# Optimization experiments

Measured on AMD Instinct MI355X. Metric: run time of the kernel, lower is better.

## Reference

```python
import jax, jax.numpy as jnp
import numpy as np

B, S, D, H = 2, 4096, 128, 128
EPS = 1e-6
NEG_INF = -1e30


def _complex_linear(xr, xi, Wr, Wi, br, bi):
    # x: (B,S,D); W: (H,D); complex linear (Wr + i Wi)(xr + i xi) + (br + i bi) per layer math:
    # real_out = (xr Wr + br) - (xi Wi + bi); imag_out = (xi Wr + br) + (xr Wi + bi)
    out_r = xr @ Wr.T + br - (xi @ Wi.T + bi)
    out_i = xi @ Wr.T + br + (xr @ Wi.T + bi)
    return out_r, out_i


def setup_inputs() -> dict:
    key = jax.random.key(0)
    ks = jax.random.split(key, 24)
    scale = 1.0 / np.sqrt(D)
    def W(k):
        return jax.random.normal(k, (H, D), jnp.float32) * scale
    def b(k):
        return jax.random.normal(k, (H,), jnp.float32) * 0.01
    inp = {
        "Z_q": jax.random.normal(ks[0], (B, 2, S, D, 1), jnp.float32),
        "Z_k": jax.random.normal(ks[1], (B, 2, S, D, 1), jnp.float32),
        "Z_v": jax.random.normal(ks[2], (B, 2, S, D, 1), jnp.float32),
        "Wq_r": W(ks[3]), "Wq_i": W(ks[4]), "bq_r": b(ks[5]), "bq_i": b(ks[6]),
        "Wk_r": W(ks[7]), "Wk_i": W(ks[8]), "bk_r": b(ks[9]), "bk_i": b(ks[10]),
        "Wv_r": W(ks[11]), "Wv_i": W(ks[12]), "bv_r": b(ks[13]), "bv_i": b(ks[14]),
        "Wp_r": W(ks[15]), "Wp_i": W(ks[16]), "bp_r": b(ks[17]), "bp_i": b(ks[18]),
        "noise_floor": jnp.asarray(1.0, jnp.float32),
        "tau": jnp.asarray(0.0, jnp.float32),
    }
    return inp


def reference(Z_q, Z_k, Z_v,
              Wq_r, Wq_i, bq_r, bq_i,
              Wk_r, Wk_i, bk_r, bk_i,
              Wv_r, Wv_i, bv_r, bv_i,
              Wp_r, Wp_i, bp_r, bp_i,
              noise_floor, tau):
    # squeeze trailing singleton; split real/imag -> (B,S,D)
    zqr, zqi = Z_q[:, 0, :, :, 0], Z_q[:, 1, :, :, 0]
    zkr, zki = Z_k[:, 0, :, :, 0], Z_k[:, 1, :, :, 0]
    zvr, zvi = Z_v[:, 0, :, :, 0], Z_v[:, 1, :, :, 0]

    Qr, Qi = _complex_linear(zqr, zqi, Wq_r, Wq_i, bq_r, bq_i)
    Kr, Ki = _complex_linear(zkr, zki, Wk_r, Wk_i, bk_r, bk_i)
    Vr, Vi = _complex_linear(zvr, zvi, Wv_r, Wv_i, bv_r, bv_i)

    # InverseMahalanobis: R2[b,i,j] = sum_h |Q[b,i]-K[b,j]|^2
    q2 = jnp.sum(Qr * Qr + Qi * Qi, axis=-1)          # (B,S)
    k2 = jnp.sum(Kr * Kr + Ki * Ki, axis=-1)          # (B,S)
    re_qk = (jnp.einsum('bsh,bth->bst', Qr, Kr)
             + jnp.einsum('bsh,bth->bst', Qi, Ki))    # (B,S,S)
    R2 = q2[:, :, None] + k2[:, None, :] - 2.0 * re_qk

    attn_scores = -jax.nn.softplus(tau) * jnp.log(noise_floor ** 2 + R2 + EPS)
    mask = jnp.tril(jnp.ones((S, S), dtype=bool))[None]
    attn_scores = jnp.where(mask, attn_scores, NEG_INF)
    attn_weights = jax.nn.softmax(attn_scores / jnp.sqrt(jnp.float32(H)), axis=-1)

    # attn (real) times complex V
    est_r = jnp.einsum('bst,bth->bsh', attn_weights, Vr)
    est_i = jnp.einsum('bst,bth->bsh', attn_weights, Vi)

    out_r, out_i = _complex_linear(est_r, est_i, Wp_r, Wp_i, bp_r, bp_i)
    out = jnp.stack((out_r, out_i), axis=1)[..., None]  # (B,2,S,H,1)
    return out, attn_weights
```

## Files before the change

kernel.cpp:

```cpp
#include <hip/hip_runtime.h>

#define S_LEN 4096
#define NBATCH 2
#define ROWS (NBATCH*S_LEN)
#define OUT_ELEMS 2097152

typedef _Float16 f16;
typedef _Float16 f16x8 __attribute__((ext_vector_type(8)));
typedef _Float16 f16x4 __attribute__((ext_vector_type(4)));
typedef float f32x4 __attribute__((ext_vector_type(4)));

#define MT_OFF    0x000000
#define BIAS_OFF  0x080000
#define SC_OFF    0x081000
#define QH_OFF    0x100000
#define KH_OFF    0x500000
#define VT_OFF    0x900000
#define Q2_OFF    0xD00000
#define K2_OFF    0xD10000
#define L_OFF     0xD20000
#define EST_OFF   0xE00000
#define WS_NEED   0x1600000

#define MFMA16(A,B,C) __builtin_amdgcn_mfma_f32_16x16x32_f16(A,B,C,0,0,0)

__device__ __forceinline__ void async_cp16(f16* lds, const f16* g) {
  __builtin_amdgcn_global_load_lds(
      (const __attribute__((address_space(1))) void*)g,
      (__attribute__((address_space(3))) void*)lds, 16, 0, 0);
}

__device__ __forceinline__ void stage16(f16* lds, const f16* g, int stride, int tid) {
#pragma unroll
  for (int i = 0; i < 2; ++i) {
    int idx = i*256 + tid;
    int row = idx >> 2, c = idx & 3;
    async_cp16(lds + idx*8, g + (size_t)row*stride + c*8);
  }
}

__device__ __forceinline__ void stage32(f16* lds, const float* g, int stride, int tid) {
#pragma unroll
  for (int i = 0; i < 4; ++i) {
    int idx = i*256 + tid;
    int row = idx >> 3, c = idx & 7;
    const float4* gp = (const float4*)(g + (size_t)row*stride + c*4);
    float4 v = *gp;
    f16x4 h; h[0]=(f16)v.x; h[1]=(f16)v.y; h[2]=(f16)v.z; h[3]=(f16)v.w;
    *(f16x4*)(lds + row*32 + c*4) = h;
  }
}

__device__ __forceinline__ void mfma_step(const f16* Asm, const f16* Bsm, int lane,
                                          int wm, int wn, f32x4 acc[4][4]) {
  f16x8 a[4], b[4];
  int rr = lane & 15, kk = (lane >> 4) << 3;
#pragma unroll
  for (int i=0;i<4;i++) a[i] = *(const f16x8*)(Asm + (wm + i*16 + rr)*32 + kk);
#pragma unroll
  for (int j=0;j<4;j++) b[j] = *(const f16x8*)(Bsm + (wn + j*16 + rr)*32 + kk);
#pragma unroll
  for (int i=0;i<4;i++)
#pragma unroll
    for (int j=0;j<4;j++) acc[i][j] = MFMA16(a[i], b[j], acc[i][j]);
}

__global__ __launch_bounds__(256)
void k_build(const float* Wqr, const float* Wqi, const float* bqr, const float* bqi,
             const float* Wkr, const float* Wki, const float* bkr, const float* bki,
             const float* Wvr, const float* Wvi, const float* bvr, const float* bvi,
             const float* Wpr, const float* Wpi, const float* bpr, const float* bpi,
             f16* Mt, float* bias) {
  int mat = blockIdx.x;
  const float *Wr, *Wi, *br, *bi;
  if (mat == 0)      { Wr=Wqr; Wi=Wqi; br=bqr; bi=bqi; }
  else if (mat == 1) { Wr=Wkr; Wi=Wki; br=bkr; bi=bki; }
  else if (mat == 2) { Wr=Wvr; Wi=Wvi; br=bvr; bi=bvi; }
  else               { Wr=Wpr; Wi=Wpi; br=bpr; bi=bpi; }
  int idx = blockIdx.y*256 + threadIdx.x;
  int n = idx >> 8, k = idx & 255;
  int d = k & 127, h = n & 127;
  float w = (k < 128) ? ((n < 128) ? Wr[h*128+d] : Wi[h*128+d])
                      : ((n < 128) ? -Wi[h*128+d] : Wr[h*128+d]);
  Mt[mat*65536 + n*256 + k] = (f16)w;
  if (k == 0)
    bias[mat*256 + n] = (n < 128) ? (br[n] - bi[n]) : (br[n-128] + bi[n-128]);
}

__global__ __launch_bounds__(256)
void k_init(float* est, float* lsum, float* sc, const float* nf, const float* tau) {
  int idx = blockIdx.x*256 + threadIdx.x;
  if (idx < 524288) ((float4*)est)[idx] = make_float4(0.f,0.f,0.f,0.f);
  else { int j = idx - 524288; if (j < 2048) ((float4*)lsum)[j] = make_float4(0.f,0.f,0.f,0.f); }
  if (idx == 0) {
    float t = tau[0];
    float c = __builtin_log2f(1.0f + __builtin_exp2f(t * 1.4426950408889634f))
              * 0.6931471805599453f;
    sc[0] = -c * 0.08838834764831845f;
    sc[1] = nf[0]*nf[0] + 1e-6f;
  }
}

__global__ __launch_bounds__(256)
void k_proj(const float* Zq, const float* Zk, const float* Zv,
            const f16* Mt, const float* bias,
            f16* Qh, f16* Kh, f16* Vt) {
  __shared__ f16 Asm[128*32];
  __shared__ f16 Bsm[128*32];
  __shared__ float bias_s[128];
  int tid = threadIdx.x;
  int mode = blockIdx.z;
  int m0 = blockIdx.x * 128, n0 = blockIdx.y * 128;
  const float* Z = (mode==0) ? Zq : (mode==1 ? Zk : Zv);
  const f16* Bt = Mt + mode*65536;
  if (tid < 128) bias_s[tid] = bias[mode*256 + n0 + tid];
  int b = m0 >> 12, s0 = m0 & 4095;
  int lane = tid & 63, w = tid >> 6;
  int wm = (w >> 1)*64, wn = (w & 1)*64;
  f32x4 acc[4][4] = {};
  for (int kb = 0; kb < 8; ++kb) {
    int k0 = kb*32;
    int part = k0 >> 7, d0 = k0 & 127;
    const float* Ag = Z + (((size_t)(b*2 + part))*S_LEN + s0)*128 + d0;
    stage32(Asm, Ag, 128, tid);
    stage16(Bsm, Bt + n0*256 + k0, 256, tid);
    __syncthreads();
    mfma_step(Asm, Bsm, lane, wm, wn, acc);
    __syncthreads();
  }
  int rr = (lane>>4)*4, cc = lane & 15;
  if (mode < 2) {
    f16* O = (mode==0) ? Qh : Kh;
#pragma unroll
    for (int i=0;i<4;i++)
#pragma unroll
      for (int j=0;j<4;j++) {
        int cl = wn + j*16 + cc;
        int cg = n0 + cl;
        float bv = bias_s[cl];
#pragma unroll
        for (int r=0;r<4;r++) {
          int rg = m0 + wm + i*16 + rr + r;
          O[(size_t)rg*256 + cg] = (f16)(acc[i][j][r] + bv);
        }
      }
  } else {
#pragma unroll
    for (int i=0;i<4;i++) {
      int t0 = s0 + wm + i*16 + rr;
#pragma unroll
      for (int j=0;j<4;j++) {
        int cl = wn + j*16 + cc;
        int cg = n0 + cl;
        float bv = bias_s[cl];
        f16x4 h4;
#pragma unroll
        for (int r=0;r<4;r++) h4[r] = (f16)(acc[i][j][r] + bv);
        *(f16x4*)(Vt + (size_t)b*1048576 + (size_t)cg*4096 + t0) = h4;
      }
    }
  }
}

__global__ __launch_bounds__(256)
void k_sq(const f16* Qh, const f16* Kh, float* q2, float* k2) {
  int w = threadIdx.x >> 6, lane = threadIdx.x & 63;
  int rid = blockIdx.x*4 + w;
  const f16* src = (rid < ROWS) ? Qh + (size_t)rid*256 : Kh + (size_t)(rid-ROWS)*256;
  f16x4 v = *(const f16x4*)(src + lane*4);
  float s = 0.f;
#pragma unroll
  for (int i=0;i<4;i++) { float f = (float)v[i]; s += f*f; }
#pragma unroll
  for (int m=32;m>=1;m>>=1) s += __shfl_xor(s, m, 64);
  if (lane==0) { if (rid < ROWS) q2[rid]=s; else k2[rid-ROWS]=s; }
}

template<int WRITE>
__global__ __launch_bounds__(256)
void k_attn(const f16* Qh, const f16* Kh, const float* q2, const float* k2,
            const float* sc, float* lsum, float* attn) {
  __shared__ f16 Asm[128*32];
  __shared__ f16 Bsm[128*32];
  __shared__ float q2s[128], k2s[128], ls[128];
  int x = blockIdx.x;
  int b = x / 528, r = x % 528;
  int sb = (int)((__builtin_sqrtf(8.f*(float)r + 1.f) - 1.f)*0.5f);
  while ((sb+1)*(sb+2)/2 <= r) sb++;
  while (sb*(sb+1)/2 > r) sb--;
  int tb = r - sb*(sb+1)/2;
  int s0 = sb*128, t0 = tb*128;
  int tid = threadIdx.x;
  if (tid < 128) {
    q2s[tid] = q2[b*S_LEN + s0 + tid];
    k2s[tid] = k2[b*S_LEN + t0 + tid];
    if (WRITE) ls[tid] = 1.0f / lsum[b*S_LEN + s0 + tid];
  }
  float kc = sc[0], nf2 = sc[1];
  int lane = tid & 63, w = tid >> 6;
  int wm = (w >> 1)*64, wn = (w & 1)*64;
  const f16* Ag = Qh + ((size_t)(b*S_LEN) + s0)*256;
  const f16* Bg = Kh + ((size_t)(b*S_LEN) + t0)*256;
  f32x4 acc[4][4] = {};
  for (int kb=0;kb<8;kb++) {
    stage16(Asm, Ag + kb*32, 256, tid);
    stage16(Bsm, Bg + kb*32, 256, tid);
    __syncthreads();
    mfma_step(Asm, Bsm, lane, wm, wn, acc);
    __syncthreads();
  }
  int rr = (lane>>4)*4, cc = lane & 15;
  bool diag = (tb == sb);
  if (WRITE) {
#pragma unroll
    for (int i=0;i<4;i++)
#pragma unroll
      for (int j=0;j<4;j++) {
        int cl = wn + j*16 + cc;
        float kv = k2s[cl];
#pragma unroll
        for (int rg=0;rg<4;rg++) {
          int rl = wm + i*16 + rr + rg;
          float xx = nf2 + q2s[rl] + kv - 2.0f*acc[i][j][rg];
          float P = __builtin_exp2f(kc * __builtin_log2f(__builtin_fmaxf(xx, 1e-6f)));
          if (diag && (t0+cl) > (s0+rl)) P = 0.f;
          attn[((size_t)(b*S_LEN) + s0 + rl)*S_LEN + t0 + cl] = P * ls[rl];
        }
      }
  } else {
    float rs[4][4];
#pragma unroll
    for (int i=0;i<4;i++)
#pragma unroll
      for (int rg=0;rg<4;rg++) rs[i][rg]=0.f;
#pragma unroll
    for (int i=0;i<4;i++)
#pragma unroll
      for (int j=0;j<4;j++) {
        int cl = wn + j*16 + cc;
        float kv = k2s[cl];
#pragma unroll
        for (int rg=0;rg<4;rg++) {
          int rl = wm + i*16 + rr + rg;
          float xx = nf2 + q2s[rl] + kv - 2.0f*acc[i][j][rg];
          float P = __builtin_exp2f(kc * __builtin_log2f(__builtin_fmaxf(xx, 1e-6f)));
          if (diag && (t0+cl) > (s0+rl)) P = 0.f;
          rs[i][rg] += P;
        }
      }
#pragma unroll
    for (int m=8;m>=1;m>>=1)
#pragma unroll
      for (int i=0;i<4;i++)
#pragma unroll
        for (int rg=0;rg<4;rg++) rs[i][rg] += __shfl_xor(rs[i][rg], m, 64);
    if (cc == 0)
#pragma unroll
      for (int i=0;i<4;i++)
#pragma unroll
        for (int rg=0;rg<4;rg++) {
          int rl = wm + i*16 + rr + rg;
          atomicAdd(&lsum[b*S_LEN + s0 + rl], rs[i][rg]);
        }
  }
}

__global__ __launch_bounds__(256)
void k_zupper(float* attn) {
  int rid = blockIdx.x;
  int b = rid >> 12, s = rid & 4095;
  int tstart = ((s >> 7) + 1) << 7;
  float4* p = (float4*)(attn + ((size_t)(b*S_LEN) + s)*S_LEN);
  for (int i = (tstart >> 2) + threadIdx.x; i < 1024; i += 256)
    p[i] = make_float4(0.f,0.f,0.f,0.f);
}

__global__ __launch_bounds__(256)
void k_pv(const float* attn, const f16* Vt, float* est) {
  __shared__ f16 Asm[128*32];
  __shared__ f16 Bsm[128*32];
  int sb = blockIdx.x, nb = blockIdx.y, z = blockIdx.z;
  int b = z >> 2, tc = z & 3;
  if (tc > (sb >> 3)) return;
  int s0 = sb*128, h0 = nb*128;
  int tid = threadIdx.x;
  int lane = tid & 63, w = tid >> 6;
  int wm = (w>>1)*64, wn = (w&1)*64;
  int tb1 = tc*8 + 8; if (tb1 > sb+1) tb1 = sb+1;
  const float* Abase = attn + ((size_t)(b*S_LEN) + s0)*S_LEN;
  const f16* Bbase = Vt + (size_t)b*1048576 + (size_t)h0*4096;
  f32x4 acc[4][4] = {};
  for (int tb = tc*8; tb < tb1; ++tb)
    for (int kk = 0; kk < 4; ++kk) {
      int t0 = tb*128 + kk*32;
      stage32(Asm, Abase + t0, S_LEN, tid);
      stage16(Bsm, Bbase + t0, 4096, tid);
      __syncthreads();
      mfma_step(Asm, Bsm, lane, wm, wn, acc);
      __syncthreads();
    }
  int rr = (lane>>4)*4, cc = lane & 15;
#pragma unroll
  for (int i=0;i<4;i++)
#pragma unroll
    for (int j=0;j<4;j++) {
      int cg = h0 + wn + j*16 + cc;
#pragma unroll
      for (int rg=0;rg<4;rg++) {
        int rgl = s0 + wm + i*16 + rr + rg;
        atomicAdd(&est[((size_t)(b*S_LEN) + rgl)*256 + cg], acc[i][j][rg]);
      }
    }
}

__global__ __launch_bounds__(256)
void k_out(const float* est, const f16* Mt, const float* bias, float* outp) {
  __shared__ f16 Asm[128*32];
  __shared__ f16 Bsm[128*32];
  __shared__ float bias_s[128];
  int m0 = blockIdx.x*128, n0 = blockIdx.y*128;
  int tid = threadIdx.x;
  if (tid < 128) bias_s[tid] = bias[3*256 + n0 + tid];
  int lane = tid & 63, w = tid >> 6;
  int wm = (w>>1)*64, wn = (w&1)*64;
  const f16* Bt = Mt + 3*65536;
  f32x4 acc[4][4] = {};
  for (int kb=0;kb<8;kb++) {
    stage32(Asm, est + (size_t)m0*256 + kb*32, 256, tid);
    stage16(Bsm, Bt + n0*256 + kb*32, 256, tid);
    __syncthreads();
    mfma_step(Asm, Bsm, lane, wm, wn, acc);
    __syncthreads();
  }
  int rr = (lane>>4)*4, cc = lane & 15;
  int b = m0 >> 12, s0 = m0 & 4095;
#pragma unroll
  for (int i=0;i<4;i++)
#pragma unroll
    for (int j=0;j<4;j++) {
      int cl = wn + j*16 + cc;
      int cg = n0 + cl;
      int comp = cg >> 7, h = cg & 127;
      float bv = bias_s[cl];
#pragma unroll
      for (int rg=0;rg<4;rg++) {
        int s = s0 + wm + i*16 + rr + rg;
        outp[(((size_t)(b*2 + comp))*S_LEN + s)*128 + h] = acc[i][j][rg] + bv;
      }
    }
}

extern "C" void kernel_launch(void* const* d_in, const int* in_sizes, int n_in,
                              void* d_out, int out_size, void* d_ws, size_t ws_size,
                              hipStream_t stream) {
  (void)in_sizes; (void)n_in; (void)out_size;
  if (ws_size < (size_t)WS_NEED) return;
  const float* Zq = (const float*)d_in[0];
  const float* Zk = (const float*)d_in[1];
  const float* Zv = (const float*)d_in[2];
  char* ws = (char*)d_ws;
  f16*   Mt   = (f16*)(ws + MT_OFF);
  float* bias = (float*)(ws + BIAS_OFF);
  float* sc   = (float*)(ws + SC_OFF);
  f16*   Qh   = (f16*)(ws + QH_OFF);
  f16*   Kh   = (f16*)(ws + KH_OFF);
  f16*   Vt   = (f16*)(ws + VT_OFF);
  float* q2   = (float*)(ws + Q2_OFF);
  float* k2   = (float*)(ws + K2_OFF);
  float* lsum = (float*)(ws + L_OFF);
  float* est  = (float*)(ws + EST_OFF);
  float* outp = (float*)d_out;
  float* attn = outp + OUT_ELEMS;

  k_build<<<dim3(4,256), 256, 0, stream>>>(
      (const float*)d_in[3],  (const float*)d_in[4],  (const float*)d_in[5],  (const float*)d_in[6],
      (const float*)d_in[7],  (const float*)d_in[8],  (const float*)d_in[9],  (const float*)d_in[10],
      (const float*)d_in[11], (const float*)d_in[12], (const float*)d_in[13], (const float*)d_in[14],
      (const float*)d_in[15], (const float*)d_in[16], (const float*)d_in[17], (const float*)d_in[18],
      Mt, bias);
  k_init<<<2056, 256, 0, stream>>>(est, lsum, sc, (const float*)d_in[19], (const float*)d_in[20]);
  k_proj<<<dim3(64,2,3), 256, 0, stream>>>(Zq, Zk, Zv, Mt, bias, Qh, Kh, Vt);
  k_sq<<<4096, 256, 0, stream>>>(Qh, Kh, q2, k2);
  k_attn<0><<<1056, 256, 0, stream>>>(Qh, Kh, q2, k2, sc, lsum, attn);
  k_attn<1><<<1056, 256, 0, stream>>>(Qh, Kh, q2, k2, sc, lsum, attn);
  k_zupper<<<8192, 256, 0, stream>>>(attn);
  k_pv<<<dim3(32,2,8), 256, 0, stream>>>(attn, Vt, est);
  k_out<<<dim3(64,2), 256, 0, stream>>>(est, Mt, bias, outp);
}
```

Before: 319.2 us.

## Single-pass attention with fp16 P workspace, fused normalization and zero-fill

Replaces the two-pass attention (sum pass plus recompute-and-write pass) with a single pass that writes unnormalized fp16 probabilities to a workspace and accumulates row sums. The PV kernel reads the fp16 P, writes the normalized fp32 attention output during staging, and the output projection applies the 1/lsum row scale. It also folds the q2/k2 norm computation into the projection epilogue via atomics and zero-fills the upper triangle inside the attention kernel. This removes one full QK^T recompute and halves the P read bandwidth, at the cost of a 64 MB workspace write/read and fp16 rounding of P before normalization.

```diff
diff --git a/kernel.cpp b/kernel.cpp
--- a/kernel.cpp
+++ b/kernel.cpp
@@ -20,7 +20,8 @@
 #define K2_OFF    0xD10000
 #define L_OFF     0xD20000
 #define EST_OFF   0xE00000
-#define WS_NEED   0x1600000
+#define PW_OFF    0x1600000
+#define WS_NEED   0x5600000
 
 #define MFMA16(A,B,C) __builtin_amdgcn_mfma_f32_16x16x32_f16(A,B,C,0,0,0)
 
@@ -39,14 +40,16 @@
   }
 }
 
-__device__ __forceinline__ void stage32(f16* lds, const float* g, int stride, int tid) {
+__device__ __forceinline__ void stage32(f16* lds, const float* g, int stride, int tid,
+                                        const float* rowscale) {
 #pragma unroll
   for (int i = 0; i < 4; ++i) {
     int idx = i*256 + tid;
     int row = idx >> 3, c = idx & 7;
     const float4* gp = (const float4*)(g + (size_t)row*stride + c*4);
     float4 v = *gp;
-    f16x4 h; h[0]=(f16)v.x; h[1]=(f16)v.y; h[2]=(f16)v.z; h[3]=(f16)v.w;
+    float sc = rowscale ? rowscale[row] : 1.0f;
+    f16x4 h; h[0]=(f16)(v.x*sc); h[1]=(f16)(v.y*sc); h[2]=(f16)(v.z*sc); h[3]=(f16)(v.w*sc);
     *(f16x4*)(lds + row*32 + c*4) = h;
   }
 }
@@ -88,10 +91,10 @@
 }
 
 __global__ __launch_bounds__(256)
-void k_init(float* est, float* lsum, float* sc, const float* nf, const float* tau) {
+void k_init(float* est, float* zreg, float* sc, const float* nf, const float* tau) {
   int idx = blockIdx.x*256 + threadIdx.x;
   if (idx < 524288) ((float4*)est)[idx] = make_float4(0.f,0.f,0.f,0.f);
-  else { int j = idx - 524288; if (j < 2048) ((float4*)lsum)[j] = make_float4(0.f,0.f,0.f,0.f); }
+  else { int j = idx - 524288; if (j < 12288) ((float4*)zreg)[j] = make_float4(0.f,0.f,0.f,0.f); }
   if (idx == 0) {
     float t = tau[0];
     float c = __builtin_log2f(1.0f + __builtin_exp2f(t * 1.4426950408889634f))
@@ -104,7 +107,7 @@
 __global__ __launch_bounds__(256)
 void k_proj(const float* Zq, const float* Zk, const float* Zv,
             const f16* Mt, const float* bias,
-            f16* Qh, f16* Kh, f16* Vt) {
+            f16* Qh, f16* Kh, f16* Vt, float* q2, float* k2) {
   __shared__ f16 Asm[128*32];
   __shared__ f16 Bsm[128*32];
   __shared__ float bias_s[128];
@@ -122,7 +125,7 @@
     int k0 = kb*32;
     int part = k0 >> 7, d0 = k0 & 127;
     const float* Ag = Z + (((size_t)(b*2 + part))*S_LEN + s0)*128 + d0;
-    stage32(Asm, Ag, 128, tid);
+    stage32(Asm, Ag, 128, tid, nullptr);
     stage16(Bsm, Bt + n0*256 + k0, 256, tid);
     __syncthreads();
     mfma_step(Asm, Bsm, lane, wm, wn, acc);
@@ -131,6 +134,11 @@
   int rr = (lane>>4)*4, cc = lane & 15;
   if (mode < 2) {
     f16* O = (mode==0) ? Qh : Kh;
+    float rs[4][4];
+#pragma unroll
+    for (int i=0;i<4;i++)
+#pragma unroll
+      for (int r=0;r<4;r++) rs[i][r]=0.f;
 #pragma unroll
     for (int i=0;i<4;i++)
 #pragma unroll
@@ -141,9 +149,28 @@
 #pragma unroll
         for (int r=0;r<4;r++) {
           int rg = m0 + wm + i*16 + rr + r;
-          O[(size_t)rg*256 + cg] = (f16)(acc[i][j][r] + bv);
+          f16 hv = (f16)(acc[i][j][r] + bv);
+          O[(size_t)rg*256 + cg] = hv;
+          float fv = (float)hv;
+          rs[i][r] += fv*fv;
         }
       }
+#pragma unroll
+    for (int m=8;m>=1;m>>=1)
+#pragma unroll
+      for (int i=0;i<4;i++)
+#pragma unroll
+        for (int r=0;r<4;r++) rs[i][r] += __shfl_xor(rs[i][r], m, 64);
+    if (cc == 0) {
+      float* T = (mode==0) ? q2 : k2;
+#pragma unroll
+      for (int i=0;i<4;i++)
+#pragma unroll
+        for (int r=0;r<4;r++) {
+          int rg = m0 + wm + i*16 + rr + r;
+          atomicAdd(&T[rg], rs[i][r]);
+        }
+    }
   } else {
 #pragma unroll
     for (int i=0;i<4;i++) {
@@ -163,38 +190,27 @@
 }
 
 __global__ __launch_bounds__(256)
-void k_sq(const f16* Qh, const f16* Kh, float* q2, float* k2) {
-  int w = threadIdx.x >> 6, lane = threadIdx.x & 63;
-  int rid = blockIdx.x*4 + w;
-  const f16* src = (rid < ROWS) ? Qh + (size_t)rid*256 : Kh + (size_t)(rid-ROWS)*256;
-  f16x4 v = *(const f16x4*)(src + lane*4);
-  float s = 0.f;
-#pragma unroll
-  for (int i=0;i<4;i++) { float f = (float)v[i]; s += f*f; }
-#pragma unroll
-  for (int m=32;m>=1;m>>=1) s += __shfl_xor(s, m, 64);
-  if (lane==0) { if (rid < ROWS) q2[rid]=s; else k2[rid-ROWS]=s; }
-}
-
-template<int WRITE>
-__global__ __launch_bounds__(256)
 void k_attn(const f16* Qh, const f16* Kh, const float* q2, const float* k2,
-            const float* sc, float* lsum, float* attn) {
+            const float* sc, float* lsum, f16* Pws, float* attn) {
+  int x = blockIdx.x;
+  int b = x >> 10, r = x & 1023;
+  int sb = r >> 5, tb = r & 31;
+  int s0 = sb*128, t0 = tb*128;
+  int tid = threadIdx.x;
+  if (tb > sb) {
+    float4 z = make_float4(0.f,0.f,0.f,0.f);
+    int row = tid >> 1, h = tid & 1;
+    float4* p = (float4*)(attn + ((size_t)(b*S_LEN) + s0 + row)*S_LEN + t0 + h*64);
+#pragma unroll
+    for (int i=0;i<16;i++) p[i] = z;
+    return;
+  }
   __shared__ f16 Asm[128*32];
   __shared__ f16 Bsm[128*32];
-  __shared__ float q2s[128], k2s[128], ls[128];
-  int x = blockIdx.x;
-  int b = x / 528, r = x % 528;
-  int sb = (int)((__builtin_sqrtf(8.f*(float)r + 1.f) - 1.f)*0.5f);
-  while ((sb+1)*(sb+2)/2 <= r) sb++;
-  while (sb*(sb+1)/2 > r) sb--;
-  int tb = r - sb*(sb+1)/2;
-  int s0 = sb*128, t0 = tb*128;
-  int tid = threadIdx.x;
+  __shared__ float q2s[128], k2s[128];
   if (tid < 128) {
     q2s[tid] = q2[b*S_LEN + s0 + tid];
     k2s[tid] = k2[b*S_LEN + t0 + tid];
-    if (WRITE) ls[tid] = 1.0f / lsum[b*S_LEN + s0 + tid];
   }
   float kc = sc[0], nf2 = sc[1];
   int lane = tid & 63, w = tid >> 6;
@@ -211,91 +227,81 @@
   }
   int rr = (lane>>4)*4, cc = lane & 15;
   bool diag = (tb == sb);
-  if (WRITE) {
+  float rs[4][4];
+#pragma unroll
+  for (int i=0;i<4;i++)
+#pragma unroll
+    for (int rg=0;rg<4;rg++) rs[i][rg]=0.f;
+#pragma unroll
+  for (int i=0;i<4;i++)
+#pragma unroll
+    for (int j=0;j<4;j++) {
+      int cl = wn + j*16 + cc;
+      float kv = k2s[cl];
+#pragma unroll
+      for (int rg=0;rg<4;rg++) {
+        int rl = wm + i*16 + rr + rg;
+        float xx = nf2 + q2s[rl] + kv - 2.0f*acc[i][j][rg];
+        float P = __builtin_exp2f(kc * __builtin_log2f(__builtin_fmaxf(xx, 1e-6f)));
+        if (diag && (t0+cl) > (s0+rl)) P = 0.f;
+        Pws[((size_t)(b*S_LEN) + s0 + rl)*S_LEN + t0 + cl] = (f16)P;
+        rs[i][rg] += P;
+      }
+    }
+#pragma unroll
+  for (int m=8;m>=1;m>>=1)
 #pragma unroll
     for (int i=0;i<4;i++)
 #pragma unroll
-      for (int j=0;j<4;j++) {
-        int cl = wn + j*16 + cc;
-        float kv = k2s[cl];
-#pragma unroll
-        for (int rg=0;rg<4;rg++) {
-          int rl = wm + i*16 + rr + rg;
-          float xx = nf2 + q2s[rl] + kv - 2.0f*acc[i][j][rg];
-          float P = __builtin_exp2f(kc * __builtin_log2f(__builtin_fmaxf(xx, 1e-6f)));
-          if (diag && (t0+cl) > (s0+rl)) P = 0.f;
-          attn[((size_t)(b*S_LEN) + s0 + rl)*S_LEN + t0 + cl] = P * ls[rl];
-        }
-      }
-  } else {
-    float rs[4][4];
+      for (int rg=0;rg<4;rg++) rs[i][rg] += __shfl_xor(rs[i][rg], m, 64);
+  if (cc == 0)
 #pragma unroll
     for (int i=0;i<4;i++)
 #pragma unroll
-      for (int rg=0;rg<4;rg++) rs[i][rg]=0.f;
-#pragma unroll
-    for (int i=0;i<4;i++)
-#pragma unroll
-      for (int j=0;j<4;j++) {
-        int cl = wn + j*16 + cc;
-        float kv = k2s[cl];
-#pragma unroll
-        for (int rg=0;rg<4;rg++) {
-          int rl = wm + i*16 + rr + rg;
-          float xx = nf2 + q2s[rl] + kv - 2.0f*acc[i][j][rg];
-          float P = __builtin_exp2f(kc * __builtin_log2f(__builtin_fmaxf(xx, 1e-6f)));
-          if (diag && (t0+cl) > (s0+rl)) P = 0.f;
-          rs[i][rg] += P;
-        }
-      }
-#pragma unroll
-    for (int m=8;m>=1;m>>=1)
-#pragma unroll
-      for (int i=0;i<4;i++)
-#pragma unroll
-        for (int rg=0;rg<4;rg++) rs[i][rg] += __shfl_xor(rs[i][rg], m, 64);
-    if (cc == 0)
-#pragma unroll
-      for (int i=0;i<4;i++)
-#pragma unroll
-        for (int rg=0;rg<4;rg++) {
-          int rl = wm + i*16 + rr + rg;
-          atomicAdd(&lsum[b*S_LEN + s0 + rl], rs[i][rg]);
-        }
-  }
-}
-
-__global__ __launch_bounds__(256)
-void k_zupper(float* attn) {
-  int rid = blockIdx.x;
-  int b = rid >> 12, s = rid & 4095;
-  int tstart = ((s >> 7) + 1) << 7;
-  float4* p = (float4*)(attn + ((size_t)(b*S_LEN) + s)*S_LEN);
-  for (int i = (tstart >> 2) + threadIdx.x; i < 1024; i += 256)
-    p[i] = make_float4(0.f,0.f,0.f,0.f);
-}
-
-__global__ __launch_bounds__(256)
-void k_pv(const float* attn, const f16* Vt, float* est) {
+      for (int rg=0;rg<4;rg++) {
+        int rl = wm + i*16 + rr + rg;
+        atomicAdd(&lsum[b*S_LEN + s0 + rl], rs[i][rg]);
+      }
+}
+
+__global__ __launch_bounds__(256)
+void k_pv(const f16* Pws, const f16* Vt, const float* lsum, float* est, float* attn) {
   __shared__ f16 Asm[128*32];
   __shared__ f16 Bsm[128*32];
-  int sb = blockIdx.x, nb = blockIdx.y, z = blockIdx.z;
-  int b = z >> 2, tc = z & 3;
-  if (tc > (sb >> 3)) return;
+  __shared__ float ls[128];
+  int r = blockIdx.x;
+  int nb = blockIdx.y, b = blockIdx.z;
+  int sb = 0;
+  while (r >= ((sb+4)>>2)) { r -= (sb+4)>>2; sb++; }
+  int c = r;
   int s0 = sb*128, h0 = nb*128;
   int tid = threadIdx.x;
+  bool wrb = (nb == 0);
+  if (wrb && tid < 128) ls[tid] = 1.0f / lsum[b*S_LEN + s0 + tid];
   int lane = tid & 63, w = tid >> 6;
   int wm = (w>>1)*64, wn = (w&1)*64;
-  int tb1 = tc*8 + 8; if (tb1 > sb+1) tb1 = sb+1;
-  const float* Abase = attn + ((size_t)(b*S_LEN) + s0)*S_LEN;
+  int tb0 = c*4, tb1 = tb0 + 4; if (tb1 > sb+1) tb1 = sb+1;
+  const f16* Abase = Pws + ((size_t)(b*S_LEN) + s0)*S_LEN;
   const f16* Bbase = Vt + (size_t)b*1048576 + (size_t)h0*4096;
   f32x4 acc[4][4] = {};
-  for (int tb = tc*8; tb < tb1; ++tb)
+  int row2 = tid >> 1, half2 = tid & 1;
+  for (int tb = tb0; tb < tb1; ++tb)
     for (int kk = 0; kk < 4; ++kk) {
       int t0 = tb*128 + kk*32;
-      stage32(Asm, Abase + t0, S_LEN, tid);
+      stage16(Asm, Abase + t0, S_LEN, tid);
       stage16(Bsm, Bbase + t0, 4096, tid);
       __syncthreads();
+      if (wrb) {
+        float invl = ls[row2];
+        const f16x8* src = (const f16x8*)(Asm + row2*32 + half2*16);
+        f16x8 v0 = src[0], v1 = src[1];
+        float4* dst = (float4*)(attn + ((size_t)(b*S_LEN) + s0 + row2)*S_LEN + t0 + half2*16);
+        float4 o;
+        o.x=(float)v0[0]*invl; o.y=(float)v0[1]*invl; o.z=(float)v0[2]*invl; o.w=(float)v0[3]*invl; dst[0]=o;
+        o.x=(float)v0[4]*invl; o.y=(float)v0[5]*invl; o.z=(float)v0[6]*invl; o.w=(float)v0[7]*invl; dst[1]=o;
+        o.x=(float)v1[0]*invl; o.y=(float)v1[1]*invl; o.z=(float)v1[2]*invl; o.w=(float)v1[3]*invl; dst[2]=o;
+        o.x=(float)v1[4]*invl; o.y=(float)v1[5]*invl; o.z=(float)v1[6]*invl; o.w=(float)v1[7]*invl; dst[3]=o;
+      }
       mfma_step(Asm, Bsm, lane, wm, wn, acc);
       __syncthreads();
     }
@@ -314,26 +320,32 @@
 }
 
 __global__ __launch_bounds__(256)
-void k_out(const float* est, const f16* Mt, const float* bias, float* outp) {
+void k_out(const float* est, const f16* Mt, const float* bias, const float* lsum,
+           float* outp) {
   __shared__ f16 Asm[128*32];
   __shared__ f16 Bsm[128*32];
   __shared__ float bias_s[128];
+  __shared__ float ls[128];
   int m0 = blockIdx.x*128, n0 = blockIdx.y*128;
   int tid = threadIdx.x;
-  if (tid < 128) bias_s[tid] = bias[3*256 + n0 + tid];
+  int b = m0 >> 12, s0 = m0 & 4095;
+  if (tid < 128) {
+    bias_s[tid] = bias[3*256 + n0 + tid];
+    ls[tid] = 1.0f / lsum[b*S_LEN + s0 + tid];
+  }
+  __syncthreads();
   int lane = tid & 63, w = tid >> 6;
   int wm = (w>>1)*64, wn = (w&1)*64;
   const f16* Bt = Mt + 3*65536;
   f32x4 acc[4][4] = {};
   for (int kb=0;kb<8;kb++) {
-    stage32(Asm, est + (size_t)m0*256 + kb*32, 256, tid);
+    stage32(Asm, est + (size_t)m0*256 + kb*32, 256, tid, ls);
     stage16(Bsm, Bt + n0*256 + kb*32, 256, tid);
     __syncthreads();
     mfma_step(Asm, Bsm, lane, wm, wn, acc);
     __syncthreads();
   }
   int rr = (lane>>4)*4, cc = lane & 15;
-  int b = m0 >> 12, s0 = m0 & 4095;
 #pragma unroll
   for (int i=0;i<4;i++)
 #pragma unroll
@@ -369,6 +381,7 @@
   float* k2   = (float*)(ws + K2_OFF);
   float* lsum = (float*)(ws + L_OFF);
   float* est  = (float*)(ws + EST_OFF);
+  f16*   Pws  = (f16*)(ws + PW_OFF);
   float* outp = (float*)d_out;
   float* attn = outp + OUT_ELEMS;
 
@@ -378,12 +391,9 @@
       (const float*)d_in[11], (const float*)d_in[12], (const float*)d_in[13], (const float*)d_in[14],
       (const float*)d_in[15], (const float*)d_in[16], (const float*)d_in[17], (const float*)d_in[18],
       Mt, bias);
-  k_init<<<2056, 256, 0, stream>>>(est, lsum, sc, (const float*)d_in[19], (const float*)d_in[20]);
-  k_proj<<<dim3(64,2,3), 256, 0, stream>>>(Zq, Zk, Zv, Mt, bias, Qh, Kh, Vt);
-  k_sq<<<4096, 256, 0, stream>>>(Qh, Kh, q2, k2);
-  k_attn<0><<<1056, 256, 0, stream>>>(Qh, Kh, q2, k2, sc, lsum, attn);
-  k_attn<1><<<1056, 256, 0, stream>>>(Qh, Kh, q2, k2, sc, lsum, attn);
-  k_zupper<<<8192, 256, 0, stream>>>(attn);
-  k_pv<<<dim3(32,2,8), 256, 0, stream>>>(attn, Vt, est);
-  k_out<<<dim3(64,2), 256, 0, stream>>>(est, Mt, bias, outp);
-}
+  k_init<<<2096, 256, 0, stream>>>(est, q2, sc, (const float*)d_in[19], (const float*)d_in[20]);
+  k_proj<<<dim3(64,2,3), 256, 0, stream>>>(Zq, Zk, Zv, Mt, bias, Qh, Kh, Vt, q2, k2);
+  k_attn<<<2048, 256, 0, stream>>>(Qh, Kh, q2, k2, sc, lsum, Pws, attn);
+  k_pv<<<dim3(144,2,2), 256, 0, stream>>>(Pws, Vt, lsum, est, attn);
+  k_out<<<dim3(64,2), 256, 0, stream>>>(est, Mt, bias, lsum, outp);
+}
```

After: 302.1 us. 5.4% less time.
